# Optimization experiments

Hardware: AMD Instinct MI355X
Metric: run time of the kernel (lower is better)

Reference implementation:

```python
import jax, jax.numpy as jnp
import numpy as np

# Fixed multi-scale geometry implied by the module's hard-coded reshapes
# (48^2=2304, 24^2=576, 12^2=144; Len_q = 576).
SPATIAL = [(48, 48), (24, 24), (12, 12)]
NH, NP, NL = 6, 4, 3  # num_heads, num_points, num_levels


def _process_reference_points(rp):
    """rp: (B, 3024, 2) normalized refs over 3 levels -> (B, 576, 2).
    Mirrors the part1/part2/part3 averaging in MSDeformAttn.forward."""
    B = rp.shape[0]
    p1 = rp[:, :2304].reshape(B, 48, 48, 2).mean(axis=(1, 2))[:, None, :]
    p1 = jnp.broadcast_to(p1, (B, 576, 2))
    p2 = rp[:, 2304:2880].reshape(B, 576, 2)
    p3 = rp[:, 2880:].reshape(B, 12, 12, 2)
    p3 = jax.image.resize(p3, (B, 24, 24, 2), 'bilinear')  # align_corners=False
    p3 = p3.reshape(B, 576, 2)
    return (p1 + p2 + p3) / 3.0


def _bilinear_sample(val_l, coords, Hl, Wl):
    """val_l: (B, Hl*Wl, nh, d) one level's values.
    coords: (B, Lq, nh, P, 2) normalized (x, y) sampling locations.
    Returns (B, Lq, P, nh, d) bilinearly sampled values (zero padding)."""
    B, Lq, nh, P, _ = coords.shape
    px = coords[..., 0] * Wl - 0.5
    py = coords[..., 1] * Hl - 0.5
    x0 = jnp.floor(px)
    y0 = jnp.floor(py)
    lx = px - x0
    ly = py - y0
    x0i = x0.astype(jnp.int32)
    y0i = y0.astype(jnp.int32)

    def _flat(a):  # (B,Lq,nh,P) -> (B,Lq*P,nh,1) matching value layout
        return a.transpose(0, 1, 3, 2).reshape(B, Lq * P, nh, 1)

    def gather(xi, yi):
        valid = (xi >= 0) & (xi < Wl) & (yi >= 0) & (yi < Hl)
        xi_c = jnp.clip(xi, 0, Wl - 1)
        yi_c = jnp.clip(yi, 0, Hl - 1)
        idx = _flat(yi_c * Wl + xi_c)
        v = jnp.take_along_axis(val_l, idx, axis=1)  # (B,Lq*P,nh,d)
        return v * _flat(valid).astype(val_l.dtype)

    w00 = _flat((1 - lx) * (1 - ly))
    w10 = _flat(lx * (1 - ly))
    w01 = _flat((1 - lx) * ly)
    w11 = _flat(lx * ly)
    out = (gather(x0i, y0i) * w00 + gather(x0i + 1, y0i) * w10 +
           gather(x0i, y0i + 1) * w01 + gather(x0i + 1, y0i + 1) * w11)
    return out.reshape(B, Lq, P, nh, -1)


def setup_inputs() -> dict:
    key = jax.random.key(0)
    ks = jax.random.split(key, 8)
    B, C = 32, 384
    Lq, Lv = 576, 3024
    # reference points exactly as get_reference_points builds them
    refs = []
    for (Hl, Wl) in SPATIAL:
        ry, rx = np.meshgrid(np.linspace(0.5, Hl - 0.5, Hl) / Hl,
                             np.linspace(0.5, Wl - 0.5, Wl) / Wl, indexing='ij')
        refs.append(np.stack([rx.ravel(), ry.ravel()], -1))
    rp = np.concatenate(refs, 0).astype(np.float32)  # (3024, 2)
    rp = np.broadcast_to(rp[None, :, None, :], (B, Lv, 1, 2)).copy()
    s = 1.0 / np.sqrt(C)
    return {
        'query': jax.random.normal(ks[0], (B, Lq, C), jnp.float32),
        'value': jax.random.normal(ks[1], (B, Lv, C), jnp.float32),
        'reference_points': jnp.asarray(rp),
        'W_value': jax.random.normal(ks[2], (C, C), jnp.float32) * s,
        'b_value': jnp.zeros((C,), jnp.float32),
        'W_off': jax.random.normal(ks[3], (C, NH * NL * NP * 2), jnp.float32) * 0.01,
        'b_off': jnp.zeros((NH * NL * NP * 2,), jnp.float32),
        'W_attn': jax.random.normal(ks[4], (C, NH * NL * NP), jnp.float32) * s,
        'b_attn': jnp.zeros((NH * NL * NP,), jnp.float32),
        'W_out': jax.random.normal(ks[5], (C, C), jnp.float32) * s,
        'b_out': jnp.zeros((C,), jnp.float32),
    }


def reference(query, value, reference_points, W_value, b_value, W_off, b_off,
              W_attn, b_attn, W_out, b_out):
    B, Lq, C = query.shape
    d = C // NH
    val = (value @ W_value + b_value).reshape(B, -1, NH, d)
    off = (query @ W_off + b_off).reshape(B, Lq, NH, NL, NP, 2)
    attn = jax.nn.softmax((query @ W_attn + b_attn)
                          .reshape(B, Lq, NH, NL * NP), axis=-1)
    attn = attn.reshape(B, Lq, NH, NL, NP)
    ref = _process_reference_points(reference_points.reshape(B, -1, 2))
    coords = off + ref[:, :, None, None, None, :]  # (B,Lq,nh,L,P,2)
    out = jnp.zeros((B, Lq, NH, d), query.dtype)
    start = 0
    for l, (Hl, Wl) in enumerate(SPATIAL):
        val_l = val[:, start:start + Hl * Wl]
        sampled = _bilinear_sample(val_l, coords[:, :, :, l], Hl, Wl)
        out = out + jnp.einsum('bqpnd,bqnp->bqnd', sampled, attn[:, :, :, l])
        start += Hl * Wl
    return out.reshape(B, Lq, NH * d) @ W_out + b_out
```

## Files before the change

kernel.cpp:

```cpp
#include <hip/hip_runtime.h>
#include <cmath>

#define B_SZ   32
#define LQ     576
#define LV     3024
#define CDIM   384
#define NHEAD  6
#define DHEAD  64
#define NLVL   3
#define NPTS   4
#define NPROJ  216

typedef short  bx4 __attribute__((ext_vector_type(4)));
typedef short  bx8 __attribute__((ext_vector_type(8)));
typedef float  fx4 __attribute__((ext_vector_type(4)));

__device__ __forceinline__ short f2bf(float f) {
    unsigned u = __builtin_bit_cast(unsigned, f);
    unsigned r = (u + 0x7FFFu + ((u >> 16) & 1u)) >> 16;
    return (short)r;
}
__device__ __forceinline__ float bf2f(unsigned short u) {
    return __builtin_bit_cast(float, ((unsigned)u) << 16);
}

__global__ __launch_bounds__(256) void cast_transpose_kernel(
    const float* __restrict__ W, short* __restrict__ Wt, int K, int N)
{
    int idx = blockIdx.x * 256 + threadIdx.x;
    if (idx >= K * N) return;
    int n = idx / K, k = idx - n * K;
    Wt[idx] = f2bf(W[(size_t)k * N + n]);
}

__global__ __launch_bounds__(256) void prep_proj_kernel(
    const float* __restrict__ W_off, const float* __restrict__ b_off,
    const float* __restrict__ W_attn, const float* __restrict__ b_attn,
    short* __restrict__ Wh, short* __restrict__ Wl, float* __restrict__ bc)
{
    int idx = blockIdx.x * 256 + threadIdx.x;
    if (idx >= NPROJ * CDIM) return;
    int n = idx / CDIM, k = idx - n * CDIM;
    float w = (n < 144) ? W_off[(size_t)k * 144 + n]
                        : W_attn[(size_t)k * 72 + (n - 144)];
    short h = f2bf(w);
    float hf = bf2f((unsigned short)h);
    Wh[idx] = h;
    Wl[idx] = f2bf(w - hf);
    if (idx < NPROJ) bc[idx] = (idx < 144) ? b_off[idx] : b_attn[idx - 144];
}

template <bool BF16_OUT>
__global__ __launch_bounds__(256) void gemm_mfma_kernel(
    const float* __restrict__ A, const short* __restrict__ Wt,
    const float* __restrict__ bias, void* __restrict__ Cout,
    int M, int N, int K)
{
    __shared__ short As[128 * 72];
    __shared__ short Bs[128 * 72];

    const int tid = threadIdx.x;
    const int m0 = blockIdx.y * 128;
    const int n0 = blockIdx.x * 128;

    const int akq = (tid & 15) << 2;
    const int am  = tid >> 4;
    const int bk8 = (tid & 7) << 3;
    const int bn  = tid >> 3;

    const int w  = tid >> 6;
    const int l  = tid & 63;
    const int mw = (w & 1) * 64;
    const int nw = (w >> 1) * 64;
    const int lr = l & 15;
    const int ko = (l >> 4) * 8;

    fx4 acc[4][4] = {};

    for (int k0 = 0; k0 < K; k0 += 64) {
        #pragma unroll
        for (int r = 0; r < 8; ++r) {
            const int m = am + r * 16;
            const float4 v = *(const float4*)(A + (size_t)(m0 + m) * K + k0 + akq);
            bx4 s;
            s[0] = f2bf(v.x); s[1] = f2bf(v.y); s[2] = f2bf(v.z); s[3] = f2bf(v.w);
            *(bx4*)&As[m * 72 + akq] = s;
        }
        #pragma unroll
        for (int r = 0; r < 4; ++r) {
            const int n = bn + r * 32;
            const bx8 wv = *(const bx8*)(Wt + (size_t)(n0 + n) * K + k0 + bk8);
            *(bx8*)&Bs[n * 72 + bk8] = wv;
        }
        __syncthreads();

        #pragma unroll
        for (int ks = 0; ks < 2; ++ks) {
            bx8 af[4], bfr[4];
            #pragma unroll
            for (int i = 0; i < 4; ++i)
                af[i] = *(const bx8*)&As[(mw + i * 16 + lr) * 72 + ks * 32 + ko];
            #pragma unroll
            for (int j = 0; j < 4; ++j)
                bfr[j] = *(const bx8*)&Bs[(nw + j * 16 + lr) * 72 + ks * 32 + ko];
            #pragma unroll
            for (int i = 0; i < 4; ++i)
                #pragma unroll
                for (int j = 0; j < 4; ++j)
                    acc[i][j] = __builtin_amdgcn_mfma_f32_16x16x32_bf16(
                        af[i], bfr[j], acc[i][j], 0, 0, 0);
        }
        __syncthreads();
    }

    const int rrow = (l >> 4) * 4;
    #pragma unroll
    for (int j = 0; j < 4; ++j) {
        const int col = n0 + nw + j * 16 + lr;
        const float bv = bias[col];
        #pragma unroll
        for (int i = 0; i < 4; ++i) {
            const int row = m0 + mw + i * 16 + rrow;
            #pragma unroll
            for (int r = 0; r < 4; ++r) {
                if (BF16_OUT)
                    ((short*)Cout)[(size_t)(row + r) * N + col] = f2bf(acc[i][j][r] + bv);
                else
                    ((float*)Cout)[(size_t)(row + r) * N + col] = acc[i][j][r] + bv;
            }
        }
    }
}

__global__ __launch_bounds__(256) void gemm_mfma_bf16A_kernel(
    const short* __restrict__ A, const short* __restrict__ Wt,
    const float* __restrict__ bias, float* __restrict__ C,
    int M, int N, int K)
{
    __shared__ short As[128 * 72];
    __shared__ short Bs[128 * 72];

    const int tid = threadIdx.x;
    const int m0 = blockIdx.y * 128;
    const int n0 = blockIdx.x * 128;

    const int k8 = (tid & 7) << 3;
    const int rr = tid >> 3;

    const int w  = tid >> 6;
    const int l  = tid & 63;
    const int mw = (w & 1) * 64;
    const int nw = (w >> 1) * 64;
    const int lr = l & 15;
    const int ko = (l >> 4) * 8;

    fx4 acc[4][4] = {};

    for (int k0 = 0; k0 < K; k0 += 64) {
        #pragma unroll
        for (int r = 0; r < 4; ++r) {
            const int m = rr + r * 32;
            *(bx8*)&As[m * 72 + k8] = *(const bx8*)(A + (size_t)(m0 + m) * K + k0 + k8);
            *(bx8*)&Bs[m * 72 + k8] = *(const bx8*)(Wt + (size_t)(n0 + m) * K + k0 + k8);
        }
        __syncthreads();

        #pragma unroll
        for (int ks = 0; ks < 2; ++ks) {
            bx8 af[4], bfr[4];
            #pragma unroll
            for (int i = 0; i < 4; ++i)
                af[i] = *(const bx8*)&As[(mw + i * 16 + lr) * 72 + ks * 32 + ko];
            #pragma unroll
            for (int j = 0; j < 4; ++j)
                bfr[j] = *(const bx8*)&Bs[(nw + j * 16 + lr) * 72 + ks * 32 + ko];
            #pragma unroll
            for (int i = 0; i < 4; ++i)
                #pragma unroll
                for (int j = 0; j < 4; ++j)
                    acc[i][j] = __builtin_amdgcn_mfma_f32_16x16x32_bf16(
                        af[i], bfr[j], acc[i][j], 0, 0, 0);
        }
        __syncthreads();
    }

    const int rrow = (l >> 4) * 4;
    #pragma unroll
    for (int j = 0; j < 4; ++j) {
        const int col = n0 + nw + j * 16 + lr;
        const float bv = bias[col];
        #pragma unroll
        for (int i = 0; i < 4; ++i) {
            const int row = m0 + mw + i * 16 + rrow;
            #pragma unroll
            for (int r = 0; r < 4; ++r)
                C[(size_t)(row + r) * N + col] = acc[i][j][r] + bv;
        }
    }
}

__global__ __launch_bounds__(256) void gemm_proj_split_kernel(
    const float* __restrict__ A, const short* __restrict__ Wh,
    const short* __restrict__ Wl, const float* __restrict__ bias,
    float* __restrict__ C, int M, int N, int K)
{
    __shared__ short Ah[128 * 40];
    __shared__ short Al[128 * 40];
    __shared__ short Bh[128 * 40];
    __shared__ short Bl[128 * 40];

    const int tid = threadIdx.x;
    const int m0 = blockIdx.y * 128;
    const int n0 = blockIdx.x * 128;

    const int kq = (tid & 7) << 2;
    const int rw = tid >> 3;

    const int w  = tid >> 6;
    const int l  = tid & 63;
    const int mw = (w & 1) * 64;
    const int nw = (w >> 1) * 64;
    const int lr = l & 15;
    const int ko = (l >> 4) * 8;

    fx4 acc[4][4] = {};

    for (int k0 = 0; k0 < K; k0 += 32) {
        #pragma unroll
        for (int r = 0; r < 4; ++r) {
            const int m = rw + r * 32;
            const float4 v = *(const float4*)(A + (size_t)(m0 + m) * K + k0 + kq);
            bx4 sh, sl;
            #pragma unroll
            for (int t = 0; t < 4; ++t) {
                const float f = ((const float*)&v)[t];
                const short h = f2bf(f);
                sh[t] = h;
                sl[t] = f2bf(f - bf2f((unsigned short)h));
            }
            *(bx4*)&Ah[m * 40 + kq] = sh;
            *(bx4*)&Al[m * 40 + kq] = sl;

            bx4 wh = {}, wl = {};
            if (n0 + m < N) {
                wh = *(const bx4*)(Wh + (size_t)(n0 + m) * K + k0 + kq);
                wl = *(const bx4*)(Wl + (size_t)(n0 + m) * K + k0 + kq);
            }
            *(bx4*)&Bh[m * 40 + kq] = wh;
            *(bx4*)&Bl[m * 40 + kq] = wl;
        }
        __syncthreads();

        bx8 ah[4], al[4], bh[4], bl[4];
        #pragma unroll
        for (int i = 0; i < 4; ++i) {
            ah[i] = *(const bx8*)&Ah[(mw + i * 16 + lr) * 40 + ko];
            al[i] = *(const bx8*)&Al[(mw + i * 16 + lr) * 40 + ko];
        }
        #pragma unroll
        for (int j = 0; j < 4; ++j) {
            bh[j] = *(const bx8*)&Bh[(nw + j * 16 + lr) * 40 + ko];
            bl[j] = *(const bx8*)&Bl[(nw + j * 16 + lr) * 40 + ko];
        }
        #pragma unroll
        for (int i = 0; i < 4; ++i)
            #pragma unroll
            for (int j = 0; j < 4; ++j) {
                acc[i][j] = __builtin_amdgcn_mfma_f32_16x16x32_bf16(al[i], bh[j], acc[i][j], 0, 0, 0);
                acc[i][j] = __builtin_amdgcn_mfma_f32_16x16x32_bf16(ah[i], bl[j], acc[i][j], 0, 0, 0);
                acc[i][j] = __builtin_amdgcn_mfma_f32_16x16x32_bf16(ah[i], bh[j], acc[i][j], 0, 0, 0);
            }
        __syncthreads();
    }

    const int rrow = (l >> 4) * 4;
    #pragma unroll
    for (int j = 0; j < 4; ++j) {
        const int col = n0 + nw + j * 16 + lr;
        if (col >= N) continue;
        const float bv = bias[col];
        #pragma unroll
        for (int i = 0; i < 4; ++i) {
            const int row = m0 + mw + i * 16 + rrow;
            #pragma unroll
            for (int r = 0; r < 4; ++r)
                C[(size_t)(row + r) * N + col] = acc[i][j][r] + bv;
        }
    }
}

__global__ __launch_bounds__(256) void ref_kernel(
    const float* __restrict__ rp, float* __restrict__ refp)
{
    const int b = blockIdx.x;
    const float* r = rp + (size_t)b * LV * 2;
    const int tid = threadIdx.x;

    __shared__ float redx[256], redy[256];
    float sx = 0.f, sy = 0.f;
    for (int i = tid; i < 2304; i += 256) {
        sx += r[2 * i + 0];
        sy += r[2 * i + 1];
    }
    redx[tid] = sx; redy[tid] = sy;
    __syncthreads();
    for (int s = 128; s > 0; s >>= 1) {
        if (tid < s) { redx[tid] += redx[tid + s]; redy[tid] += redy[tid + s]; }
        __syncthreads();
    }
    const float p1x = redx[0] * (1.f / 2304.f);
    const float p1y = redy[0] * (1.f / 2304.f);

    const float* g = r + 2880 * 2;
    for (int q = tid; q < 576; q += 256) {
        const float p2x = r[(2304 + q) * 2 + 0];
        const float p2y = r[(2304 + q) * 2 + 1];
        const int qy = q / 24, qx = q % 24;
        const float syc = fminf(fmaxf(0.5f * qy - 0.25f, 0.f), 11.f);
        const float sxc = fminf(fmaxf(0.5f * qx - 0.25f, 0.f), 11.f);
        int y0 = min((int)syc, 10);
        int x0 = min((int)sxc, 10);
        const float fy = syc - (float)y0, fx = sxc - (float)x0;
        const float v00x = g[(y0 * 12 + x0) * 2 + 0],     v00y = g[(y0 * 12 + x0) * 2 + 1];
        const float v10x = g[(y0 * 12 + x0 + 1) * 2 + 0], v10y = g[(y0 * 12 + x0 + 1) * 2 + 1];
        const float v01x = g[((y0 + 1) * 12 + x0) * 2 + 0],     v01y = g[((y0 + 1) * 12 + x0) * 2 + 1];
        const float v11x = g[((y0 + 1) * 12 + x0 + 1) * 2 + 0], v11y = g[((y0 + 1) * 12 + x0 + 1) * 2 + 1];
        const float p3x = (1.f - fy) * ((1.f - fx) * v00x + fx * v10x)
                        + fy * ((1.f - fx) * v01x + fx * v11x);
        const float p3y = (1.f - fy) * ((1.f - fx) * v00y + fx * v10y)
                        + fy * ((1.f - fx) * v01y + fx * v11y);
        refp[((size_t)b * LQ + q) * 2 + 0] = (p1x + p2x + p3x) * (1.f / 3.f);
        refp[((size_t)b * LQ + q) * 2 + 1] = (p1y + p2y + p3y) * (1.f / 3.f);
    }
}

__global__ __launch_bounds__(384) void sample_kernel(
    const unsigned short* __restrict__ val, const float* __restrict__ proj,
    const float* __restrict__ refp, short* __restrict__ mid)
{
    const int i = blockIdx.x;
    const int g = i & 7;
    const int r = i >> 3;
    const int b = g * 4 + (r / LQ);
    const int q = r - (r / LQ) * LQ;
    const int bq = b * LQ + q;
    const int tid = threadIdx.x;

    __shared__ float attn[72];
    __shared__ int   sloc[72][4];
    __shared__ float swt[72][4];

    if (tid < 72) {
        attn[tid] = proj[(size_t)bq * NPROJ + 144 + tid];

        const int h = tid / 12;
        const int rr = tid % 12;
        const int l = rr >> 2;
        const int p = rr & 3;

        const int HL[3] = {48, 24, 12};
        const int ST[3] = {0, 2304, 2880};
        const int Hl = HL[l], Wl = HL[l], st = ST[l];

        const float rx = refp[bq * 2 + 0];
        const float ry = refp[bq * 2 + 1];
        const int oc = ((h * NLVL + l) * NPTS + p) * 2;
        const float cx = proj[(size_t)bq * NPROJ + oc + 0] + rx;
        const float cy = proj[(size_t)bq * NPROJ + oc + 1] + ry;

        const float px = cx * (float)Wl - 0.5f;
        const float py = cy * (float)Hl - 0.5f;
        const float x0f = floorf(px), y0f = floorf(py);
        const float lx = px - x0f, ly = py - y0f;
        const int x0 = (int)x0f, y0 = (int)y0f;

        #pragma unroll
        for (int k = 0; k < 4; ++k) {
            const int dx = k & 1, dy = k >> 1;
            const int xi = x0 + dx, yi = y0 + dy;
            const bool v = (xi >= 0) && (xi < Wl) && (yi >= 0) && (yi < Hl);
            const int xc = min(max(xi, 0), Wl - 1);
            const int yc = min(max(yi, 0), Hl - 1);
            sloc[tid][k] = st + yc * Wl + xc;
            const float wx = dx ? lx : 1.f - lx;
            const float wy = dy ? ly : 1.f - ly;
            swt[tid][k] = v ? wx * wy : 0.f;
        }
    }
    __syncthreads();

    if (tid < NHEAD) {
        float mx = -1e30f;
        #pragma unroll
        for (int j = 0; j < 12; ++j) mx = fmaxf(mx, attn[tid * 12 + j]);
        float s = 0.f;
        #pragma unroll
        for (int j = 0; j < 12; ++j) {
            const float e = expf(attn[tid * 12 + j] - mx);
            attn[tid * 12 + j] = e;
            s += e;
        }
        const float inv = 1.f / s;
        #pragma unroll
        for (int j = 0; j < 12; ++j) attn[tid * 12 + j] *= inv;
    }
    __syncthreads();

    const int h = tid >> 6;
    const int c = tid & 63;
    const unsigned short* vb = val + (size_t)b * LV * CDIM + h * DHEAD + c;
    float acc = 0.f;
    #pragma unroll
    for (int s = 0; s < 12; ++s) {
        const int j = h * 12 + s;
        const float a = attn[j];
        const float sum = swt[j][0] * bf2f(vb[(size_t)sloc[j][0] * CDIM])
                        + swt[j][1] * bf2f(vb[(size_t)sloc[j][1] * CDIM])
                        + swt[j][2] * bf2f(vb[(size_t)sloc[j][2] * CDIM])
                        + swt[j][3] * bf2f(vb[(size_t)sloc[j][3] * CDIM]);
        acc += a * sum;
    }
    mid[(size_t)bq * CDIM + tid] = f2bf(acc);
}

extern "C" void kernel_launch(void* const* d_in, const int* in_sizes, int n_in,
                              void* d_out, int out_size, void* d_ws, size_t ws_size,
                              hipStream_t stream)
{
    (void)in_sizes; (void)n_in; (void)out_size; (void)ws_size;

    const float* query   = (const float*)d_in[0];
    const float* value   = (const float*)d_in[1];
    const float* rp      = (const float*)d_in[2];
    const float* W_value = (const float*)d_in[3];
    const float* b_value = (const float*)d_in[4];
    const float* W_off   = (const float*)d_in[5];
    const float* b_off   = (const float*)d_in[6];
    const float* W_attn  = (const float*)d_in[7];
    const float* b_attn  = (const float*)d_in[8];
    const float* W_out   = (const float*)d_in[9];
    const float* b_out   = (const float*)d_in[10];
    float* out = (float*)d_out;

    char* p = (char*)d_ws;
    auto take = [&](size_t bytes) { char* q = p; p += (bytes + 255) & ~(size_t)255; return q; };
    short* val  = (short*)take((size_t)B_SZ * LV * CDIM * 2);
    short* mid  = (short*)take((size_t)B_SZ * LQ * CDIM * 2);
    short* Wt   = (short*)take((size_t)CDIM * CDIM * 2);
    short* Wh   = (short*)take((size_t)NPROJ * CDIM * 2);
    short* Wl   = (short*)take((size_t)NPROJ * CDIM * 2);
    float* proj = (float*)take((size_t)B_SZ * LQ * NPROJ * 4);
    float* refp = (float*)take((size_t)B_SZ * LQ * 2 * 4);
    float* bc   = (float*)take((size_t)NPROJ * 4);

    const int Mv = B_SZ * LV;
    const int Mq = B_SZ * LQ;

    cast_transpose_kernel<<<(CDIM * CDIM + 255) / 256, 256, 0, stream>>>(
        W_value, Wt, CDIM, CDIM);
    gemm_mfma_kernel<true><<<dim3(CDIM / 128, Mv / 128), 256, 0, stream>>>(
        value, Wt, b_value, val, Mv, CDIM, CDIM);
    prep_proj_kernel<<<(NPROJ * CDIM + 255) / 256, 256, 0, stream>>>(
        W_off, b_off, W_attn, b_attn, Wh, Wl, bc);
    gemm_proj_split_kernel<<<dim3((NPROJ + 127) / 128, Mq / 128), 256, 0, stream>>>(
        query, Wh, Wl, bc, proj, Mq, NPROJ, CDIM);
    ref_kernel<<<B_SZ, 256, 0, stream>>>(rp, refp);
    sample_kernel<<<Mq, 384, 0, stream>>>(
        (const unsigned short*)val, proj, refp, mid);
    cast_transpose_kernel<<<(CDIM * CDIM + 255) / 256, 256, 0, stream>>>(
        W_out, Wt, CDIM, CDIM);
    gemm_mfma_bf16A_kernel<<<dim3(CDIM / 128, Mq / 128), 256, 0, stream>>>(
        mid, Wt, b_out, out, Mq, CDIM, CDIM);
}
```

Measured before the change: 435.6 us.

## Use full-N 128x384 tiles for value and output projection GEMMs

Replaces the 128x128-tiled GEMM kernels with one templated kernel in which each 512-thread block computes a 128-row by full-384-column tile. The fp32 value input (and the bf16 mid input) is then read and converted only once, where before it was read three times, once per N tile. In exchange the kernel uses more LDS (about 73KB) and more accumulator registers per wave, which lowers occupancy, and it launches fewer blocks. The two transposed weight buffers are also split so they no longer share one workspace slot.

Result: faster. 425.7 us (-2.3%).

```diff
diff --git a/kernel.cpp b/kernel.cpp
--- a/kernel.cpp
+++ b/kernel.cpp
@@ -50,63 +50,73 @@
     if (idx < NPROJ) bc[idx] = (idx < 144) ? b_off[idx] : b_attn[idx - 144];
 }
 
-template <bool BF16_OUT>
-__global__ __launch_bounds__(256) void gemm_mfma_kernel(
-    const float* __restrict__ A, const short* __restrict__ Wt,
+template <bool A_FP32, bool OUT_BF16>
+__global__ __launch_bounds__(512) void gemm_fullN_kernel(
+    const void* __restrict__ Av, const short* __restrict__ Wt,
     const float* __restrict__ bias, void* __restrict__ Cout,
-    int M, int N, int K)
-{
+    int M, int K)
+{
+    constexpr int N = 384;
     __shared__ short As[128 * 72];
-    __shared__ short Bs[128 * 72];
+    __shared__ short Bs[384 * 72];
 
     const int tid = threadIdx.x;
-    const int m0 = blockIdx.y * 128;
-    const int n0 = blockIdx.x * 128;
-
-    const int akq = (tid & 15) << 2;
-    const int am  = tid >> 4;
-    const int bk8 = (tid & 7) << 3;
-    const int bn  = tid >> 3;
+    const int m0 = blockIdx.x * 128;
 
     const int w  = tid >> 6;
     const int l  = tid & 63;
-    const int mw = (w & 1) * 64;
-    const int nw = (w >> 1) * 64;
+    const int wr = (w & 1) * 64;
+    const int wc = (w >> 1) * 96;
     const int lr = l & 15;
     const int ko = (l >> 4) * 8;
 
-    fx4 acc[4][4] = {};
+    fx4 acc[4][6] = {};
 
     for (int k0 = 0; k0 < K; k0 += 64) {
-        #pragma unroll
-        for (int r = 0; r < 8; ++r) {
-            const int m = am + r * 16;
-            const float4 v = *(const float4*)(A + (size_t)(m0 + m) * K + k0 + akq);
-            bx4 s;
-            s[0] = f2bf(v.x); s[1] = f2bf(v.y); s[2] = f2bf(v.z); s[3] = f2bf(v.w);
-            *(bx4*)&As[m * 72 + akq] = s;
-        }
-        #pragma unroll
-        for (int r = 0; r < 4; ++r) {
-            const int n = bn + r * 32;
-            const bx8 wv = *(const bx8*)(Wt + (size_t)(n0 + n) * K + k0 + bk8);
-            *(bx8*)&Bs[n * 72 + bk8] = wv;
+        if (A_FP32) {
+            const float* A = (const float*)Av;
+            #pragma unroll
+            for (int r = 0; r < 4; ++r) {
+                const int id = tid + r * 512;
+                const int m  = id >> 4;
+                const int kq = (id & 15) << 2;
+                const float4 v = *(const float4*)(A + (size_t)(m0 + m) * K + k0 + kq);
+                bx4 s;
+                s[0] = f2bf(v.x); s[1] = f2bf(v.y); s[2] = f2bf(v.z); s[3] = f2bf(v.w);
+                *(bx4*)&As[m * 72 + kq] = s;
+            }
+        } else {
+            const short* A = (const short*)Av;
+            #pragma unroll
+            for (int r = 0; r < 2; ++r) {
+                const int id = tid + r * 512;
+                const int m  = id >> 3;
+                const int k8 = (id & 7) << 3;
+                *(bx8*)&As[m * 72 + k8] = *(const bx8*)(A + (size_t)(m0 + m) * K + k0 + k8);
+            }
+        }
+        #pragma unroll
+        for (int r = 0; r < 6; ++r) {
+            const int id = tid + r * 512;
+            const int n  = id >> 3;
+            const int k8 = (id & 7) << 3;
+            *(bx8*)&Bs[n * 72 + k8] = *(const bx8*)(Wt + (size_t)n * K + k0 + k8);
         }
         __syncthreads();
 
         #pragma unroll
         for (int ks = 0; ks < 2; ++ks) {
-            bx8 af[4], bfr[4];
+            bx8 af[4], bfr[6];
             #pragma unroll
             for (int i = 0; i < 4; ++i)
-                af[i] = *(const bx8*)&As[(mw + i * 16 + lr) * 72 + ks * 32 + ko];
-            #pragma unroll
-            for (int j = 0; j < 4; ++j)
-                bfr[j] = *(const bx8*)&Bs[(nw + j * 16 + lr) * 72 + ks * 32 + ko];
+                af[i] = *(const bx8*)&As[(wr + i * 16 + lr) * 72 + ks * 32 + ko];
+            #pragma unroll
+            for (int j = 0; j < 6; ++j)
+                bfr[j] = *(const bx8*)&Bs[(wc + j * 16 + lr) * 72 + ks * 32 + ko];
             #pragma unroll
             for (int i = 0; i < 4; ++i)
                 #pragma unroll
-                for (int j = 0; j < 4; ++j)
+                for (int j = 0; j < 6; ++j)
                     acc[i][j] = __builtin_amdgcn_mfma_f32_16x16x32_bf16(
                         af[i], bfr[j], acc[i][j], 0, 0, 0);
         }
@@ -115,86 +125,19 @@
 
     const int rrow = (l >> 4) * 4;
     #pragma unroll
-    for (int j = 0; j < 4; ++j) {
-        const int col = n0 + nw + j * 16 + lr;
+    for (int j = 0; j < 6; ++j) {
+        const int col = wc + j * 16 + lr;
         const float bv = bias[col];
         #pragma unroll
         for (int i = 0; i < 4; ++i) {
-            const int row = m0 + mw + i * 16 + rrow;
+            const int row = m0 + wr + i * 16 + rrow;
             #pragma unroll
             for (int r = 0; r < 4; ++r) {
-                if (BF16_OUT)
+                if (OUT_BF16)
                     ((short*)Cout)[(size_t)(row + r) * N + col] = f2bf(acc[i][j][r] + bv);
                 else
                     ((float*)Cout)[(size_t)(row + r) * N + col] = acc[i][j][r] + bv;
             }
-        }
-    }
-}
-
-__global__ __launch_bounds__(256) void gemm_mfma_bf16A_kernel(
-    const short* __restrict__ A, const short* __restrict__ Wt,
-    const float* __restrict__ bias, float* __restrict__ C,
-    int M, int N, int K)
-{
-    __shared__ short As[128 * 72];
-    __shared__ short Bs[128 * 72];
-
-    const int tid = threadIdx.x;
-    const int m0 = blockIdx.y * 128;
-    const int n0 = blockIdx.x * 128;
-
-    const int k8 = (tid & 7) << 3;
-    const int rr = tid >> 3;
-
-    const int w  = tid >> 6;
-    const int l  = tid & 63;
-    const int mw = (w & 1) * 64;
-    const int nw = (w >> 1) * 64;
-    const int lr = l & 15;
-    const int ko = (l >> 4) * 8;
-
-    fx4 acc[4][4] = {};
-
-    for (int k0 = 0; k0 < K; k0 += 64) {
-        #pragma unroll
-        for (int r = 0; r < 4; ++r) {
-            const int m = rr + r * 32;
-            *(bx8*)&As[m * 72 + k8] = *(const bx8*)(A + (size_t)(m0 + m) * K + k0 + k8);
-            *(bx8*)&Bs[m * 72 + k8] = *(const bx8*)(Wt + (size_t)(n0 + m) * K + k0 + k8);
-        }
-        __syncthreads();
-
-        #pragma unroll
-        for (int ks = 0; ks < 2; ++ks) {
-            bx8 af[4], bfr[4];
-            #pragma unroll
-            for (int i = 0; i < 4; ++i)
-                af[i] = *(const bx8*)&As[(mw + i * 16 + lr) * 72 + ks * 32 + ko];
-            #pragma unroll
-            for (int j = 0; j < 4; ++j)
-                bfr[j] = *(const bx8*)&Bs[(nw + j * 16 + lr) * 72 + ks * 32 + ko];
-            #pragma unroll
-            for (int i = 0; i < 4; ++i)
-                #pragma unroll
-                for (int j = 0; j < 4; ++j)
-                    acc[i][j] = __builtin_amdgcn_mfma_f32_16x16x32_bf16(
-                        af[i], bfr[j], acc[i][j], 0, 0, 0);
-        }
-        __syncthreads();
-    }
-
-    const int rrow = (l >> 4) * 4;
-    #pragma unroll
-    for (int j = 0; j < 4; ++j) {
-        const int col = n0 + nw + j * 16 + lr;
-        const float bv = bias[col];
-        #pragma unroll
-        for (int i = 0; i < 4; ++i) {
-            const int row = m0 + mw + i * 16 + rrow;
-            #pragma unroll
-            for (int r = 0; r < 4; ++r)
-                C[(size_t)(row + r) * N + col] = acc[i][j][r] + bv;
         }
     }
 }
@@ -446,7 +389,8 @@
     auto take = [&](size_t bytes) { char* q = p; p += (bytes + 255) & ~(size_t)255; return q; };
     short* val  = (short*)take((size_t)B_SZ * LV * CDIM * 2);
     short* mid  = (short*)take((size_t)B_SZ * LQ * CDIM * 2);
-    short* Wt   = (short*)take((size_t)CDIM * CDIM * 2);
+    short* Wtv  = (short*)take((size_t)CDIM * CDIM * 2);
+    short* Wto  = (short*)take((size_t)CDIM * CDIM * 2);
     short* Wh   = (short*)take((size_t)NPROJ * CDIM * 2);
     short* Wl   = (short*)take((size_t)NPROJ * CDIM * 2);
     float* proj = (float*)take((size_t)B_SZ * LQ * NPROJ * 4);
@@ -457,9 +401,9 @@
     const int Mq = B_SZ * LQ;
 
     cast_transpose_kernel<<<(CDIM * CDIM + 255) / 256, 256, 0, stream>>>(
-        W_value, Wt, CDIM, CDIM);
-    gemm_mfma_kernel<true><<<dim3(CDIM / 128, Mv / 128), 256, 0, stream>>>(
-        value, Wt, b_value, val, Mv, CDIM, CDIM);
+        W_value, Wtv, CDIM, CDIM);
+    gemm_fullN_kernel<true, true><<<Mv / 128, 512, 0, stream>>>(
+        value, Wtv, b_value, val, Mv, CDIM);
     prep_proj_kernel<<<(NPROJ * CDIM + 255) / 256, 256, 0, stream>>>(
         W_off, b_off, W_attn, b_attn, Wh, Wl, bc);
     gemm_proj_split_kernel<<<dim3((NPROJ + 127) / 128, Mq / 128), 256, 0, stream>>>(
@@ -468,7 +412,7 @@
     sample_kernel<<<Mq, 384, 0, stream>>>(
         (const unsigned short*)val, proj, refp, mid);
     cast_transpose_kernel<<<(CDIM * CDIM + 255) / 256, 256, 0, stream>>>(
-        W_out, Wt, CDIM, CDIM);
-    gemm_mfma_bf16A_kernel<<<dim3(CDIM / 128, Mq / 128), 256, 0, stream>>>(
-        mid, Wt, b_out, out, Mq, CDIM, CDIM);
-}
+        W_out, Wto, CDIM, CDIM);
+    gemm_fullN_kernel<false, false><<<Mq / 128, 512, 0, stream>>>(
+        mid, Wto, b_out, out, Mq, CDIM);
+}
```
